# Optimization experiments

Hardware: AMD Instinct MI355X
Metric: run time of the kernel (lower is better)

The kernel has to match this reference:

```python
import jax, jax.numpy as jnp
import numpy as np

G = 8            # tile grid (8x8)
BINS = 256
CLIP_LIMIT = 4.0
H = W = 4096


def setup_inputs() -> dict:
    key = jax.random.key(0)
    k1, k2 = jax.random.split(key)
    img = jax.random.uniform(k1, (3, H, W), dtype=jnp.float32)
    # torch code draws alpha ~ U(0.5, 1.0) per tile; we pass raw U(0,1) and rescale inside
    alphas = jax.random.uniform(k2, (G * G,), dtype=jnp.float32)
    return {"img": img, "alphas": alphas}


def _to_tiles(x, hs, ws):
    # [h, w] -> [G*G, hs, ws]
    return x.reshape(G, hs, G, ws).transpose(0, 2, 1, 3).reshape(G * G, hs, ws)


def _from_tiles(t, h, w, hs, ws):
    # [G*G, hs, ws] -> [h, w]
    return t.reshape(G, G, hs, ws).transpose(0, 2, 1, 3).reshape(h, w)


def reference(img, alphas):
    c, h, w = img.shape
    hs, ws = h // G, w // G
    n_tiles = G * G
    alpha = (0.5 + 0.5 * alphas)[:, None, None]  # U(0.5,1) per tile

    lum = jnp.mean(img, axis=0)                  # [h, w]
    tiles = _to_tiles(lum, hs, ws)               # [64, hs, ws]

    # per-tile 256-bin histogram over [0,1] (torch.histc semantics: v=1 -> last bin)
    bin_idx = jnp.clip((tiles * BINS).astype(jnp.int32), 0, BINS - 1)
    flat_idx = (jnp.arange(n_tiles, dtype=jnp.int32)[:, None, None] * BINS + bin_idx).reshape(-1)
    hist = jax.ops.segment_sum(
        jnp.ones(flat_idx.shape, jnp.float32), flat_idx, num_segments=n_tiles * BINS
    ).reshape(n_tiles, BINS)

    # clip + uniform redistribution of excess
    cl = float(max(1, int(CLIP_LIMIT * hs * ws / BINS)))
    excess = jnp.sum(jnp.maximum(hist - cl, 0.0), axis=1, keepdims=True)
    hist = jnp.minimum(hist, cl) + excess / BINS

    cdf = jnp.cumsum(hist, axis=1)
    cdf = cdf / cdf[:, -1:]                      # [64, 256]

    tmin = tiles.min(axis=(1, 2), keepdims=True)
    tmax = tiles.max(axis=(1, 2), keepdims=True)
    valid = tmin < tmax                          # [64, 1, 1]

    norm = (tiles - tmin) / jnp.where(valid, tmax - tmin, 1.0)
    idx = jnp.clip((norm * 255.0).astype(jnp.int32), 0, 255)
    enhanced = cdf[jnp.arange(n_tiles)[:, None, None], idx]   # gather remap
    enhanced = alpha * enhanced + (1.0 - alpha) * tiles

    enh_full = _from_tiles(enhanced, h, w, hs, ws)            # [h, w]
    valid_full = _from_tiles(jnp.broadcast_to(valid, (n_tiles, hs, ws)), h, w, hs, ws)

    # per-channel color ratio: img/lum where lum > 1e-5 else 1 (safe division)
    nz = lum > 1e-5
    safe_lum = jnp.where(nz, lum, 1.0)
    ratio = jnp.where(nz[None], img / safe_lum[None], 1.0)    # [3, h, w]

    out = jnp.where(valid_full[None], enh_full[None] * ratio, img)
    return jnp.clip(out, 0.0, 1.0)
```

## Files before the change

kernel.cpp:

```cpp
#include <hip/hip_runtime.h>

#define HH 4096
#define WW 4096
#define TS 512
#define NBINS 256
#define NT 64
#define PLANE (HH * WW)

typedef float vf4 __attribute__((ext_vector_type(4)));

__device__ __forceinline__ float wred_min(float v) {
#pragma unroll
    for (int o = 32; o > 0; o >>= 1) v = fminf(v, __shfl_down(v, o, 64));
    return v;
}
__device__ __forceinline__ float wred_max(float v) {
#pragma unroll
    for (int o = 32; o > 0; o >>= 1) v = fmaxf(v, __shfl_down(v, o, 64));
    return v;
}
__device__ __forceinline__ float wred_sum(float v) {
#pragma unroll
    for (int o = 32; o > 0; o >>= 1) v += __shfl_down(v, o, 64);
    return v;
}

#define HIST_LANE(comp)                                              \
    {                                                                \
        float l = (a.comp + b.comp + c.comp) / 3.0f;                 \
        vmin = fminf(vmin, l);                                       \
        vmax = fmaxf(vmax, l);                                       \
        int bb = (int)(l * 256.0f);                                  \
        bb = bb < 0 ? 0 : (bb > 255 ? 255 : bb);                     \
        atomicAdd(&sh[bb], 1u);                                      \
    }

__global__ __launch_bounds__(256) void k_hist(const float* __restrict__ img,
                                              unsigned* __restrict__ ghist,
                                              unsigned* __restrict__ minu,
                                              unsigned* __restrict__ maxu) {
    __shared__ unsigned sh[NBINS];
    __shared__ float smin[4], smax[4];
    int tid = threadIdx.x;
    sh[tid] = 0u;
    __syncthreads();

    int bx = blockIdx.x;
    int t = bx >> 5;
    int chunk = bx & 31;
    int row0 = (t >> 3) * TS + chunk * 16;
    int cb4 = (t & 7) * (TS / 4);

    const float4* p0 = (const float4*)(img);
    const float4* p1 = (const float4*)(img + PLANE);
    const float4* p2 = (const float4*)(img + 2 * PLANE);

    int colv = tid & 127;
    int rsub = tid >> 7;
    float vmin = 1e30f, vmax = -1e30f;

#pragma unroll
    for (int it = 0; it < 8; ++it) {
        int r = row0 + (it << 1) + rsub;
        size_t idx4 = (size_t)r * (WW / 4) + cb4 + colv;
        float4 a = p0[idx4];
        float4 b = p1[idx4];
        float4 c = p2[idx4];
        HIST_LANE(x)
        HIST_LANE(y)
        HIST_LANE(z)
        HIST_LANE(w)
    }

    float wmn = wred_min(vmin), wmx = wred_max(vmax);
    if ((tid & 63) == 0) { smin[tid >> 6] = wmn; smax[tid >> 6] = wmx; }
    __syncthreads();
    if (tid == 0) {
        float m = fminf(fminf(smin[0], smin[1]), fminf(smin[2], smin[3]));
        float M = fmaxf(fmaxf(smax[0], smax[1]), fmaxf(smax[2], smax[3]));
        atomicMax(&minu[t], 0x3F800000u - __float_as_uint(m));
        atomicMax(&maxu[t], __float_as_uint(M));
    }
    atomicAdd(&ghist[t * NBINS + tid], sh[tid]);
}

__global__ __launch_bounds__(256) void k_cdf(const unsigned* __restrict__ ghist,
                                             const unsigned* __restrict__ minu,
                                             const unsigned* __restrict__ maxu,
                                             const float* __restrict__ alphas,
                                             float* __restrict__ cdfa,
                                             float* __restrict__ params) {
    __shared__ float sdata[NBINS];
    __shared__ float wsums[4];
    int t = blockIdx.x, tid = threadIdx.x;

    float h = (float)ghist[t * NBINS + tid];
    const float cl = 4096.0f;

    float ex = fmaxf(h - cl, 0.0f);
    float w = wred_sum(ex);
    if ((tid & 63) == 0) wsums[tid >> 6] = w;
    __syncthreads();
    float excess = wsums[0] + wsums[1] + wsums[2] + wsums[3];

    float hc = fminf(h, cl) + excess / 256.0f;

    sdata[tid] = hc;
    __syncthreads();
#pragma unroll
    for (int off = 1; off < NBINS; off <<= 1) {
        float v = (tid >= off) ? sdata[tid - off] : 0.0f;
        __syncthreads();
        sdata[tid] += v;
        __syncthreads();
    }
    float cdf = sdata[tid];
    float total = sdata[NBINS - 1];

    float alpha = 0.5f + 0.5f * alphas[t];
    cdfa[t * NBINS + tid] = alpha * (cdf / total);

    if (tid == 0) {
        float tmin = __uint_as_float(0x3F800000u - minu[t]);
        float tmax = __uint_as_float(maxu[t]);
        bool valid = tmin < tmax;
        params[t * 4 + 0] = tmin;
        params[t * 4 + 1] = valid ? (tmax - tmin) : 1.0f;
        params[t * 4 + 2] = 1.0f - alpha;
        params[t * 4 + 3] = valid ? 1.0f : 0.0f;
    }
}

#define APPLY_LANE(comp)                                             \
    {                                                                \
        float l = (a.comp + b.comp + c.comp) / 3.0f;                 \
        float nrm = (l - tp.x) / tp.y;                               \
        int ix = (int)(nrm * 255.0f);                                \
        ix = ix < 0 ? 0 : (ix > 255 ? 255 : ix);                     \
        float enh = ct[ix] + tp.z * l;                               \
        float e0, e1, e2;                                            \
        if (l > 1e-5f) {                                             \
            float rinv = enh / l;                                    \
            e0 = a.comp * rinv;                                      \
            e1 = b.comp * rinv;                                      \
            e2 = c.comp * rinv;                                      \
        } else {                                                     \
            e0 = enh; e1 = enh; e2 = enh;                            \
        }                                                            \
        if (tp.w == 0.0f) { e0 = a.comp; e1 = b.comp; e2 = c.comp; } \
        r0.comp = fminf(fmaxf(e0, 0.0f), 1.0f);                      \
        r1.comp = fminf(fmaxf(e1, 0.0f), 1.0f);                      \
        r2.comp = fminf(fmaxf(e2, 0.0f), 1.0f);                      \
    }

__global__ __launch_bounds__(256) void k_apply(const float* __restrict__ img,
                                               float* __restrict__ out,
                                               const float* __restrict__ cdfa,
                                               const float* __restrict__ params) {
    const float4* p0 = (const float4*)(img);
    const float4* p1 = (const float4*)(img + PLANE);
    const float4* p2 = (const float4*)(img + 2 * PLANE);
    vf4* o0 = (vf4*)(out);
    vf4* o1 = (vf4*)(out + PLANE);
    vf4* o2 = (vf4*)(out + 2 * PLANE);

    const int nvec = PLANE / 4;
    int stride = gridDim.x * blockDim.x;
    for (int j = blockIdx.x * blockDim.x + threadIdx.x; j < nvec; j += stride) {
        int p = j << 2;
        int hh = p >> 12;
        int wq = p & 4095;
        int t = ((hh >> 9) << 3) | (wq >> 9);
        float4 tp = ((const float4*)params)[t];
        const float* ct = cdfa + (t << 8);

        float4 a = p0[j];
        float4 b = p1[j];
        float4 c = p2[j];
        float4 r0, r1, r2;
        APPLY_LANE(x)
        APPLY_LANE(y)
        APPLY_LANE(z)
        APPLY_LANE(w)
        vf4 v0 = {r0.x, r0.y, r0.z, r0.w};
        vf4 v1 = {r1.x, r1.y, r1.z, r1.w};
        vf4 v2 = {r2.x, r2.y, r2.z, r2.w};
        __builtin_nontemporal_store(v0, &o0[j]);
        __builtin_nontemporal_store(v1, &o1[j]);
        __builtin_nontemporal_store(v2, &o2[j]);
    }
}

extern "C" void kernel_launch(void* const* d_in, const int* in_sizes, int n_in,
                              void* d_out, int out_size, void* d_ws, size_t ws_size,
                              hipStream_t stream) {
    const float* img = (const float*)d_in[0];
    const float* alphas = (const float*)d_in[1];
    float* out = (float*)d_out;

    unsigned* hist = (unsigned*)d_ws;
    unsigned* minu = hist + NT * NBINS;
    unsigned* maxu = minu + NT;
    unsigned* cnt = maxu + NT;
    float* cdfa = (float*)(cnt + NT);
    float* params = cdfa + NT * NBINS;

    (void)hipMemsetAsync(d_ws, 0, (size_t)(NT * NBINS + 3 * NT) * 4, stream);
    k_hist<<<2048, 256, 0, stream>>>(img, hist, minu, maxu);
    k_cdf<<<NT, NBINS, 0, stream>>>(hist, minu, maxu, alphas, cdfa, params);
    k_apply<<<2048, 256, 0, stream>>>(img, out, cdfa, params);
}
```

Measured before the change: 103.7 us.

## Replace global histogram atomics with per-block partials reduced in CDF kernel

The histogram kernel now writes per-block partial histograms and per-block min/max to workspace instead of using global atomics. The CDF kernel sums the 32 partials per tile and reduces min/max, which removes the memset launch. Two shared sub-histograms, split by wave parity, reduce LDS atomic contention, and a wave-shuffle scan replaces the barrier-heavy shared-memory scan. The old atomic path is kept as a fallback for when the workspace is too small; the new path needs about 2 MB of workspace.

```diff
diff --git a/kernel.cpp b/kernel.cpp
--- a/kernel.cpp
+++ b/kernel.cpp
@@ -5,6 +5,8 @@
 #define TS 512
 #define NBINS 256
 #define NT 64
+#define NCHUNK 32
+#define NBLK (NT * NCHUNK)
 #define PLANE (HH * WW)
 
 typedef float vf4 __attribute__((ext_vector_type(4)));
@@ -24,6 +26,7 @@
     for (int o = 32; o > 0; o >>= 1) v += __shfl_down(v, o, 64);
     return v;
 }
+
 
 #define HIST_LANE(comp)                                              \
     {                                                                \
@@ -35,15 +38,18 @@
         atomicAdd(&sh[bb], 1u);                                      \
     }
 
-__global__ __launch_bounds__(256) void k_hist(const float* __restrict__ img,
-                                              unsigned* __restrict__ ghist,
-                                              unsigned* __restrict__ minu,
-                                              unsigned* __restrict__ maxu) {
-    __shared__ unsigned sh[NBINS];
+__global__ __launch_bounds__(256) void k_hist_p(const float* __restrict__ img,
+                                                unsigned* __restrict__ part,
+                                                float* __restrict__ pmin,
+                                                float* __restrict__ pmax) {
+    __shared__ unsigned sh0[NBINS], sh1[NBINS];
     __shared__ float smin[4], smax[4];
     int tid = threadIdx.x;
-    sh[tid] = 0u;
-    __syncthreads();
+    sh0[tid] = 0u;
+    sh1[tid] = 0u;
+    __syncthreads();
+
+    unsigned* sh = ((tid >> 6) & 1) ? sh1 : sh0;
 
     int bx = blockIdx.x;
     int t = bx >> 5;
@@ -76,46 +82,157 @@
     if ((tid & 63) == 0) { smin[tid >> 6] = wmn; smax[tid >> 6] = wmx; }
     __syncthreads();
     if (tid == 0) {
+        pmin[bx] = fminf(fminf(smin[0], smin[1]), fminf(smin[2], smin[3]));
+        pmax[bx] = fmaxf(fmaxf(smax[0], smax[1]), fmaxf(smax[2], smax[3]));
+    }
+    part[(size_t)bx * NBINS + tid] = sh0[tid] + sh1[tid];
+}
+
+__global__ __launch_bounds__(256) void k_cdf_p(const unsigned* __restrict__ part,
+                                               const float* __restrict__ pmin,
+                                               const float* __restrict__ pmax,
+                                               const float* __restrict__ alphas,
+                                               float* __restrict__ cdfa,
+                                               float* __restrict__ params) {
+    __shared__ float wtot[4];
+    __shared__ float wsums[4];
+    __shared__ float sminmax[2];
+    int t = blockIdx.x, tid = threadIdx.x;
+
+    float h = 0.0f;
+#pragma unroll
+    for (int c = 0; c < NCHUNK; ++c)
+        h += (float)part[((size_t)(t * NCHUNK + c)) * NBINS + tid];
+
+    const float cl = 4096.0f;
+
+    float ex = fmaxf(h - cl, 0.0f);
+    float w = wred_sum(ex);
+    if ((tid & 63) == 0) wsums[tid >> 6] = w;
+
+    if (tid < 64) {
+        float m = (tid < NCHUNK) ? pmin[t * NCHUNK + tid] : 1e30f;
+        float M = (tid < NCHUNK) ? pmax[t * NCHUNK + tid] : -1e30f;
+        m = wred_min(m);
+        M = wred_max(M);
+        if (tid == 0) { sminmax[0] = m; sminmax[1] = M; }
+    }
+    __syncthreads();
+    float excess = wsums[0] + wsums[1] + wsums[2] + wsums[3];
+
+    float hc = fminf(h, cl) + excess / 256.0f;
+
+    int lane = tid & 63, wv = tid >> 6;
+    float v = hc;
+#pragma unroll
+    for (int off = 1; off < 64; off <<= 1) {
+        float u = __shfl_up(v, off, 64);
+        if (lane >= off) v += u;
+    }
+    if (lane == 63) wtot[wv] = v;
+    __syncthreads();
+    float base = 0.0f;
+    if (wv > 0) base += wtot[0];
+    if (wv > 1) base += wtot[1];
+    if (wv > 2) base += wtot[2];
+    float cdf = base + v;
+    float total = ((wtot[0] + wtot[1]) + wtot[2]) + wtot[3];
+
+    float alpha = 0.5f + 0.5f * alphas[t];
+    cdfa[t * NBINS + tid] = alpha * (cdf / total);
+
+    if (tid == 0) {
+        float tmin = sminmax[0];
+        float tmax = sminmax[1];
+        bool valid = tmin < tmax;
+        params[t * 4 + 0] = tmin;
+        params[t * 4 + 1] = valid ? (tmax - tmin) : 1.0f;
+        params[t * 4 + 2] = 1.0f - alpha;
+        params[t * 4 + 3] = valid ? 1.0f : 0.0f;
+    }
+}
+
+
+__global__ __launch_bounds__(256) void k_hist_a(const float* __restrict__ img,
+                                                unsigned* __restrict__ ghist,
+                                                unsigned* __restrict__ minu,
+                                                unsigned* __restrict__ maxu) {
+    __shared__ unsigned sh[NBINS];
+    __shared__ float smin[4], smax[4];
+    int tid = threadIdx.x;
+    sh[tid] = 0u;
+    __syncthreads();
+    unsigned* sh_ = sh;
+#define sh sh_
+    int bx = blockIdx.x;
+    int t = bx >> 5;
+    int chunk = bx & 31;
+    int row0 = (t >> 3) * TS + chunk * 16;
+    int cb4 = (t & 7) * (TS / 4);
+    const float4* p0 = (const float4*)(img);
+    const float4* p1 = (const float4*)(img + PLANE);
+    const float4* p2 = (const float4*)(img + 2 * PLANE);
+    int colv = tid & 127;
+    int rsub = tid >> 7;
+    float vmin = 1e30f, vmax = -1e30f;
+#pragma unroll
+    for (int it = 0; it < 8; ++it) {
+        int r = row0 + (it << 1) + rsub;
+        size_t idx4 = (size_t)r * (WW / 4) + cb4 + colv;
+        float4 a = p0[idx4];
+        float4 b = p1[idx4];
+        float4 c = p2[idx4];
+        HIST_LANE(x)
+        HIST_LANE(y)
+        HIST_LANE(z)
+        HIST_LANE(w)
+    }
+#undef sh
+    float wmn = wred_min(vmin), wmx = wred_max(vmax);
+    if ((tid & 63) == 0) { smin[tid >> 6] = wmn; smax[tid >> 6] = wmx; }
+    __syncthreads();
+    if (tid == 0) {
         float m = fminf(fminf(smin[0], smin[1]), fminf(smin[2], smin[3]));
         float M = fmaxf(fmaxf(smax[0], smax[1]), fmaxf(smax[2], smax[3]));
         atomicMax(&minu[t], 0x3F800000u - __float_as_uint(m));
         atomicMax(&maxu[t], __float_as_uint(M));
     }
-    atomicAdd(&ghist[t * NBINS + tid], sh[tid]);
-}
-
-__global__ __launch_bounds__(256) void k_cdf(const unsigned* __restrict__ ghist,
-                                             const unsigned* __restrict__ minu,
-                                             const unsigned* __restrict__ maxu,
-                                             const float* __restrict__ alphas,
-                                             float* __restrict__ cdfa,
-                                             float* __restrict__ params) {
-    __shared__ float sdata[NBINS];
+    atomicAdd(&ghist[t * NBINS + tid], sh_[tid]);
+}
+
+__global__ __launch_bounds__(256) void k_cdf_a(const unsigned* __restrict__ ghist,
+                                               const unsigned* __restrict__ minu,
+                                               const unsigned* __restrict__ maxu,
+                                               const float* __restrict__ alphas,
+                                               float* __restrict__ cdfa,
+                                               float* __restrict__ params) {
+    __shared__ float wtot[4];
     __shared__ float wsums[4];
     int t = blockIdx.x, tid = threadIdx.x;
-
     float h = (float)ghist[t * NBINS + tid];
     const float cl = 4096.0f;
-
     float ex = fmaxf(h - cl, 0.0f);
     float w = wred_sum(ex);
     if ((tid & 63) == 0) wsums[tid >> 6] = w;
     __syncthreads();
     float excess = wsums[0] + wsums[1] + wsums[2] + wsums[3];
-
     float hc = fminf(h, cl) + excess / 256.0f;
 
-    sdata[tid] = hc;
-    __syncthreads();
-#pragma unroll
-    for (int off = 1; off < NBINS; off <<= 1) {
-        float v = (tid >= off) ? sdata[tid - off] : 0.0f;
-        __syncthreads();
-        sdata[tid] += v;
-        __syncthreads();
-    }
-    float cdf = sdata[tid];
-    float total = sdata[NBINS - 1];
+    int lane = tid & 63, wv = tid >> 6;
+    float v = hc;
+#pragma unroll
+    for (int off = 1; off < 64; off <<= 1) {
+        float u = __shfl_up(v, off, 64);
+        if (lane >= off) v += u;
+    }
+    if (lane == 63) wtot[wv] = v;
+    __syncthreads();
+    float base = 0.0f;
+    if (wv > 0) base += wtot[0];
+    if (wv > 1) base += wtot[1];
+    if (wv > 2) base += wtot[2];
+    float cdf = base + v;
+    float total = ((wtot[0] + wtot[1]) + wtot[2]) + wtot[3];
 
     float alpha = 0.5f + 0.5f * alphas[t];
     cdfa[t * NBINS + tid] = alpha * (cdf / total);
@@ -130,6 +247,7 @@
         params[t * 4 + 3] = valid ? 1.0f : 0.0f;
     }
 }
+
 
 #define APPLY_LANE(comp)                                             \
     {                                                                \
@@ -198,15 +316,28 @@
     const float* alphas = (const float*)d_in[1];
     float* out = (float*)d_out;
 
-    unsigned* hist = (unsigned*)d_ws;
-    unsigned* minu = hist + NT * NBINS;
-    unsigned* maxu = minu + NT;
-    unsigned* cnt = maxu + NT;
-    float* cdfa = (float*)(cnt + NT);
-    float* params = cdfa + NT * NBINS;
-
-    (void)hipMemsetAsync(d_ws, 0, (size_t)(NT * NBINS + 3 * NT) * 4, stream);
-    k_hist<<<2048, 256, 0, stream>>>(img, hist, minu, maxu);
-    k_cdf<<<NT, NBINS, 0, stream>>>(hist, minu, maxu, alphas, cdfa, params);
-    k_apply<<<2048, 256, 0, stream>>>(img, out, cdfa, params);
-}
+    const size_t need = ((size_t)NBLK * NBINS + 2 * NBLK + NT * NBINS + NT * 4) * 4;
+
+    if (ws_size >= need) {
+        unsigned* part = (unsigned*)d_ws;
+        float* pmin = (float*)(part + (size_t)NBLK * NBINS);
+        float* pmax = pmin + NBLK;
+        float* cdfa = pmax + NBLK;
+        float* params = cdfa + NT * NBINS;
+
+        k_hist_p<<<NBLK, 256, 0, stream>>>(img, part, pmin, pmax);
+        k_cdf_p<<<NT, NBINS, 0, stream>>>(part, pmin, pmax, alphas, cdfa, params);
+        k_apply<<<2048, 256, 0, stream>>>(img, out, cdfa, params);
+    } else {
+        unsigned* hist = (unsigned*)d_ws;
+        unsigned* minu = hist + NT * NBINS;
+        unsigned* maxu = minu + NT;
+        float* cdfa = (float*)(maxu + 2 * NT);
+        float* params = cdfa + NT * NBINS;
+
+        (void)hipMemsetAsync(d_ws, 0, (size_t)(NT * NBINS + 3 * NT) * 4, stream);
+        k_hist_a<<<NBLK, 256, 0, stream>>>(img, hist, minu, maxu);
+        k_cdf_a<<<NT, NBINS, 0, stream>>>(hist, minu, maxu, alphas, cdfa, params);
+        k_apply<<<2048, 256, 0, stream>>>(img, out, cdfa, params);
+    }
+}
```

After: 96.55 us. 6.9% less time.
